# Kernel optimization log

Hardware: AMD Instinct MI355X
Metric: run time of the kernel (lower is better)

The kernel has to match this reference:

```python
import jax, jax.numpy as jnp
import numpy as np

BLOCK = 4096  # bitsandbytes blockwise-quantization block size


def setup_inputs() -> dict:
    key = jax.random.key(0)
    k_x, k_w, k_a, k_c, k_b = jax.random.split(key, 5)
    out_features, in_features = 16384, 4096
    numel = out_features * in_features
    x = jax.random.normal(k_x, (2, 2048, in_features), dtype=jnp.float32)
    # int8 codes stored as indices into the 256-entry dequant table
    qweight = jax.random.randint(k_w, (out_features, in_features), 0, 256, dtype=jnp.int32)
    absmax = jax.random.uniform(k_a, (numel // BLOCK,), dtype=jnp.float32)
    code = jax.random.normal(k_c, (256,), dtype=jnp.float32)
    bias = jax.random.normal(k_b, (out_features,), dtype=jnp.float32)
    return {"x": x, "qweight": qweight, "absmax": absmax, "code": code, "bias": bias}


def reference(x, qweight, absmax, code, bias):
    # dequantize_blockwise: w[i] = code[q[i]] * absmax[i // BLOCK]
    out_f, in_f = qweight.shape
    w = (code[qweight.reshape(-1)].reshape(-1, BLOCK) * absmax[:, None]).reshape(out_f, in_f)
    # F.linear(x, W, b) = x @ W^T + b
    return jnp.einsum("bsi,oi->bso", x, w) + bias
```

## Files before the change

kernel.cpp:

```cpp
#include <hip/hip_runtime.h>
#include <hip/hip_bf16.h>


typedef __bf16 bf16x8 __attribute__((ext_vector_type(8)));
typedef float  f32x4  __attribute__((ext_vector_type(4)));

#define GLD_LDS(gp, lp) \
    __builtin_amdgcn_global_load_lds((const __attribute__((address_space(1))) void*)(gp), \
                                     (__attribute__((address_space(3))) void*)(lp), 16, 0, 0)

static constexpr int M = 4096;
static constexpr int N = 16384;
static constexpr int K = 4096;
static constexpr int BM = 256;
static constexpr int BN = 256;
static constexpr int BK = 64;
static constexpr int NT = K / BK;
static constexpr int LDS_BYTES = 131072;

__global__ __launch_bounds__(256) void dequant_w(const int4* __restrict__ q4,
                                                 const float* __restrict__ code,
                                                 const float* __restrict__ absmax,
                                                 bf16x8* __restrict__ W)
{
    __shared__ float lc[256];
    lc[threadIdx.x] = code[threadIdx.x];
    __syncthreads();
    const unsigned total  = (unsigned)((unsigned long long)N * K / 8);
    const unsigned stride = gridDim.x * 256u;
    for (unsigned gid = blockIdx.x * 256u + threadIdx.x; gid < total; gid += stride) {
        int4 q0 = q4[2u * gid];
        int4 q1 = q4[2u * gid + 1u];
        float am = absmax[gid >> 9];
        bf16x8 w;
        w[0] = (__bf16)(lc[q0.x] * am);
        w[1] = (__bf16)(lc[q0.y] * am);
        w[2] = (__bf16)(lc[q0.z] * am);
        w[3] = (__bf16)(lc[q0.w] * am);
        w[4] = (__bf16)(lc[q1.x] * am);
        w[5] = (__bf16)(lc[q1.y] * am);
        w[6] = (__bf16)(lc[q1.z] * am);
        w[7] = (__bf16)(lc[q1.w] * am);
        W[gid] = w;
    }
}

__global__ __launch_bounds__(256) void cvt_x(const float4* __restrict__ x,
                                             bf16x8* __restrict__ xb)
{
    const unsigned total  = (unsigned)((unsigned long long)M * K / 8);
    const unsigned stride = gridDim.x * 256u;
    for (unsigned gid = blockIdx.x * 256u + threadIdx.x; gid < total; gid += stride) {
        float4 a = x[2u * gid];
        float4 b = x[2u * gid + 1u];
        bf16x8 o;
        o[0] = (__bf16)a.x; o[1] = (__bf16)a.y; o[2] = (__bf16)a.z; o[3] = (__bf16)a.w;
        o[4] = (__bf16)b.x; o[5] = (__bf16)b.y; o[6] = (__bf16)b.z; o[7] = (__bf16)b.w;
        xb[gid] = o;
    }
}


template<int MH, int NH>
__device__ __forceinline__ void mfma_quad(f32x4 (&acc)[8][4],
                                          const bf16x8 (&af)[4][2],
                                          const bf16x8 (&bf)[2][2])
{
    __builtin_amdgcn_s_setprio(1);
#pragma unroll
    for (int kk = 0; kk < 2; ++kk)
#pragma unroll
        for (int mi = 0; mi < 4; ++mi)
#pragma unroll
            for (int ni = 0; ni < 2; ++ni)
                acc[MH * 4 + mi][NH * 2 + ni] = __builtin_amdgcn_mfma_f32_16x16x32_bf16(
                    af[mi][kk], bf[ni][kk], acc[MH * 4 + mi][NH * 2 + ni], 0, 0, 0);
    __builtin_amdgcn_s_setprio(0);
}

__global__ __launch_bounds__(512, 2) void gemm_bt_bias(const __bf16* __restrict__ A,
                                                       const __bf16* __restrict__ B,
                                                       const float* __restrict__ bias,
                                                       float* __restrict__ C)
{
    extern __shared__ char lds[];
    const int tid  = threadIdx.x;
    const int lane = tid & 63;
    const int wave = tid >> 6;
    const int wm = wave >> 2;
    const int wn = wave & 3;

    const int cpx  = (int)gridDim.x >> 3;
    const int flat = ((int)blockIdx.x & 7) * cpx + ((int)blockIdx.x >> 3);
    const int bm = (flat & (M / BM - 1)) * BM;
    const int bn = (flat / (M / BM)) * BN;

    const int r0 = tid >> 3;
    const int cs = (tid & 7) ^ (r0 & 7);
    const int b_r0 = (r0 & 31) + (r0 >> 5) * 64;

    const __bf16* ag = A + (size_t)(bm + r0) * K + cs * 8;
    const __bf16* bg = B + (size_t)(bn + b_r0) * K + cs * 8;

    char* const ldsA0 = lds;
    char* const ldsB0 = lds + 32768;
    char* const ldsA1 = lds + 65536;
    char* const ldsB1 = lds + 98304;
    const int ldst = tid * 16;

    auto stageA = [&](char* dst, int h, size_t kn) {
        GLD_LDS(ag + kn + (size_t)(h * 64) * K,       dst + h * 16384 + ldst);
        GLD_LDS(ag + kn + (size_t)(h * 64 + 128) * K, dst + h * 16384 + 8192 + ldst);
    };
    auto stageB = [&](char* dst, int h, size_t kn) {
        GLD_LDS(bg + kn + (size_t)(h * 32) * K,       dst + h * 16384 + ldst);
        GLD_LDS(bg + kn + (size_t)(h * 32 + 128) * K, dst + h * 16384 + 8192 + ldst);
    };

    const int fr  = lane & 15;
    const int swz = ((lane >> 4) ^ (lane & 7)) << 4;
    const int aoff = (wm * 64 + fr) * 128 + swz;
    const int boff = (wn * 32 + fr) * 128 + swz;

    auto loadA = [&](const char* cA, int mh, bf16x8 (&af)[4][2]) {
        const int base = mh * 16384 + aoff;
#pragma unroll
        for (int mi = 0; mi < 4; ++mi) {
            af[mi][0] = *(const bf16x8*)(cA + (base + mi * 2048));
            af[mi][1] = *(const bf16x8*)(cA + ((base + mi * 2048) ^ 64));
        }
    };
    auto loadB = [&](const char* cB, int nh, bf16x8 (&bf)[2][2]) {
        const int base = nh * 16384 + boff;
#pragma unroll
        for (int ni = 0; ni < 2; ++ni) {
            bf[ni][0] = *(const bf16x8*)(cB + (base + ni * 2048));
            bf[ni][1] = *(const bf16x8*)(cB + ((base + ni * 2048) ^ 64));
        }
    };

    f32x4 acc[8][4] = {};

    stageA(ldsA0, 0, 0);
    stageB(ldsB0, 0, 0);
    stageB(ldsB0, 1, 0);
    stageA(ldsA0, 1, 0);
    asm volatile("s_waitcnt vmcnt(4)" ::: "memory");
    __builtin_amdgcn_s_barrier();

    auto tile_body = [&](const char* cA, const char* cB, char* nA, char* nB,
                         bool pf, size_t kn) {
        bf16x8 af[4][2], bf[2][2];
        if (pf) stageA(nA, 0, kn);
        loadA(cA, 0, af);
        loadB(cB, 0, bf);
        if (pf) asm volatile("s_waitcnt vmcnt(4)" ::: "memory");
        else    asm volatile("s_waitcnt vmcnt(0)" ::: "memory");
        __builtin_amdgcn_s_barrier();
        mfma_quad<0, 0>(acc, af, bf);
        if (pf) stageB(nB, 0, kn);
        loadB(cB, 1, bf);
        if (pf) {
            asm volatile("s_waitcnt vmcnt(4)" ::: "memory");
            __builtin_amdgcn_s_barrier();
        }
        mfma_quad<0, 1>(acc, af, bf);
        if (pf) stageB(nB, 1, kn);
        loadA(cA, 1, af);
        loadB(cB, 0, bf);
        if (pf) {
            asm volatile("s_waitcnt vmcnt(4)" ::: "memory");
            __builtin_amdgcn_s_barrier();
        }
        mfma_quad<1, 0>(acc, af, bf);
        if (pf) stageA(nA, 1, kn);
        loadB(cB, 1, bf);
        if (pf) {
            asm volatile("s_waitcnt vmcnt(4)" ::: "memory");
            __builtin_amdgcn_s_barrier();
        }
        mfma_quad<1, 1>(acc, af, bf);
    };

    for (int t = 0; t < NT; t += 2) {
        tile_body(ldsA0, ldsB0, ldsA1, ldsB1, true,        (size_t)(t + 1) * BK);
        tile_body(ldsA1, ldsB1, ldsA0, ldsB0, t + 2 < NT,  (size_t)(t + 2) * BK);
    }

    const int cn = lane & 15;
    const int rq = (lane >> 4) * 4;
#pragma unroll
    for (int ni = 0; ni < 4; ++ni) {
        const int n = bn + wn * 64 + ni * 16 + cn;
        const float bv = bias[n];
#pragma unroll
        for (int mi = 0; mi < 8; ++mi) {
#pragma unroll
            for (int r = 0; r < 4; ++r) {
                const int m = bm + wm * 128 + mi * 16 + rq + r;
                C[(size_t)m * N + n] = acc[mi][ni][r] + bv;
            }
        }
    }
}

extern "C" void kernel_launch(void* const* d_in, const int* in_sizes, int n_in,
                              void* d_out, int out_size, void* d_ws, size_t ws_size,
                              hipStream_t stream)
{
    const float* x      = (const float*)d_in[0];
    const int*   qw     = (const int*)d_in[1];
    const float* absmax = (const float*)d_in[2];
    const float* code   = (const float*)d_in[3];
    const float* bias   = (const float*)d_in[4];
    float* out = (float*)d_out;

    __bf16* Wb = (__bf16*)d_ws;
    __bf16* Xb = (__bf16*)((char*)d_ws + (size_t)N * K * sizeof(__bf16));

    static bool attr_set = false;
    if (!attr_set) {
        (void)hipFuncSetAttribute((const void*)gemm_bt_bias,
                                  hipFuncAttributeMaxDynamicSharedMemorySize, LDS_BYTES);
        attr_set = true;
    }

    dequant_w<<<2048, 256, 0, stream>>>((const int4*)qw, code, absmax, (bf16x8*)Wb);
    cvt_x<<<2048, 256, 0, stream>>>((const float4*)x, (bf16x8*)Xb);

    gemm_bt_bias<<<dim3((M / BM) * (N / BN)), dim3(512), LDS_BYTES, stream>>>(
        Xb, Wb, bias, out);
}
```

Measured before the change: 994.1 us.

## Restructure GEMM tile pipeline with fewer barriers and one-shot elementwise kernels

The GEMM main loop now loads all B fragments for a tile once, then iterates over A halves and k-slices issuing 16 MFMAs per group. This cuts the barriers per tile from four to two and reorders the global-to-LDS staging (B first, then A), with sched_barrier fences to pin the instruction order. The dequant and convert kernels drop their grid-stride loops in favor of one thread per 8-element chunk launched over the full problem size. Holding B fragments in registers raises register pressure, and the changed vmcnt wait counts must still cover the data each phase reads from LDS.

After: 992.6 us. No clear change (-0.2%).

```diff
diff --git a/kernel.cpp b/kernel.cpp
--- a/kernel.cpp
+++ b/kernel.cpp
@@ -26,57 +26,34 @@
     __shared__ float lc[256];
     lc[threadIdx.x] = code[threadIdx.x];
     __syncthreads();
-    const unsigned total  = (unsigned)((unsigned long long)N * K / 8);
-    const unsigned stride = gridDim.x * 256u;
-    for (unsigned gid = blockIdx.x * 256u + threadIdx.x; gid < total; gid += stride) {
-        int4 q0 = q4[2u * gid];
-        int4 q1 = q4[2u * gid + 1u];
-        float am = absmax[gid >> 9];
-        bf16x8 w;
-        w[0] = (__bf16)(lc[q0.x] * am);
-        w[1] = (__bf16)(lc[q0.y] * am);
-        w[2] = (__bf16)(lc[q0.z] * am);
-        w[3] = (__bf16)(lc[q0.w] * am);
-        w[4] = (__bf16)(lc[q1.x] * am);
-        w[5] = (__bf16)(lc[q1.y] * am);
-        w[6] = (__bf16)(lc[q1.z] * am);
-        w[7] = (__bf16)(lc[q1.w] * am);
-        W[gid] = w;
-    }
+    unsigned gid = blockIdx.x * 256u + threadIdx.x;
+    int4 q0 = q4[2u * gid];
+    int4 q1 = q4[2u * gid + 1u];
+    float am = absmax[gid >> 9];
+    bf16x8 w;
+    w[0] = (__bf16)(lc[q0.x] * am);
+    w[1] = (__bf16)(lc[q0.y] * am);
+    w[2] = (__bf16)(lc[q0.z] * am);
+    w[3] = (__bf16)(lc[q0.w] * am);
+    w[4] = (__bf16)(lc[q1.x] * am);
+    w[5] = (__bf16)(lc[q1.y] * am);
+    w[6] = (__bf16)(lc[q1.z] * am);
+    w[7] = (__bf16)(lc[q1.w] * am);
+    W[gid] = w;
 }
 
 __global__ __launch_bounds__(256) void cvt_x(const float4* __restrict__ x,
                                              bf16x8* __restrict__ xb)
 {
-    const unsigned total  = (unsigned)((unsigned long long)M * K / 8);
-    const unsigned stride = gridDim.x * 256u;
-    for (unsigned gid = blockIdx.x * 256u + threadIdx.x; gid < total; gid += stride) {
-        float4 a = x[2u * gid];
-        float4 b = x[2u * gid + 1u];
-        bf16x8 o;
-        o[0] = (__bf16)a.x; o[1] = (__bf16)a.y; o[2] = (__bf16)a.z; o[3] = (__bf16)a.w;
-        o[4] = (__bf16)b.x; o[5] = (__bf16)b.y; o[6] = (__bf16)b.z; o[7] = (__bf16)b.w;
-        xb[gid] = o;
-    }
-}
-
-
-template<int MH, int NH>
-__device__ __forceinline__ void mfma_quad(f32x4 (&acc)[8][4],
-                                          const bf16x8 (&af)[4][2],
-                                          const bf16x8 (&bf)[2][2])
-{
-    __builtin_amdgcn_s_setprio(1);
-#pragma unroll
-    for (int kk = 0; kk < 2; ++kk)
-#pragma unroll
-        for (int mi = 0; mi < 4; ++mi)
-#pragma unroll
-            for (int ni = 0; ni < 2; ++ni)
-                acc[MH * 4 + mi][NH * 2 + ni] = __builtin_amdgcn_mfma_f32_16x16x32_bf16(
-                    af[mi][kk], bf[ni][kk], acc[MH * 4 + mi][NH * 2 + ni], 0, 0, 0);
-    __builtin_amdgcn_s_setprio(0);
-}
+    unsigned gid = blockIdx.x * 256u + threadIdx.x;
+    float4 a = x[2u * gid];
+    float4 b = x[2u * gid + 1u];
+    bf16x8 o;
+    o[0] = (__bf16)a.x; o[1] = (__bf16)a.y; o[2] = (__bf16)a.z; o[3] = (__bf16)a.w;
+    o[4] = (__bf16)b.x; o[5] = (__bf16)b.y; o[6] = (__bf16)b.z; o[7] = (__bf16)b.w;
+    xb[gid] = o;
+}
+
 
 __global__ __launch_bounds__(512, 2) void gemm_bt_bias(const __bf16* __restrict__ A,
                                                        const __bf16* __restrict__ B,
@@ -122,69 +99,73 @@
     const int aoff = (wm * 64 + fr) * 128 + swz;
     const int boff = (wn * 32 + fr) * 128 + swz;
 
-    auto loadA = [&](const char* cA, int mh, bf16x8 (&af)[4][2]) {
+    auto loadA = [&](const char* cA, int mh, int kk, bf16x8 (&af)[4]) {
         const int base = mh * 16384 + aoff;
 #pragma unroll
-        for (int mi = 0; mi < 4; ++mi) {
-            af[mi][0] = *(const bf16x8*)(cA + (base + mi * 2048));
-            af[mi][1] = *(const bf16x8*)(cA + ((base + mi * 2048) ^ 64));
-        }
-    };
-    auto loadB = [&](const char* cB, int nh, bf16x8 (&bf)[2][2]) {
-        const int base = nh * 16384 + boff;
-#pragma unroll
-        for (int ni = 0; ni < 2; ++ni) {
-            bf[ni][0] = *(const bf16x8*)(cB + (base + ni * 2048));
-            bf[ni][1] = *(const bf16x8*)(cB + ((base + ni * 2048) ^ 64));
-        }
+        for (int mi = 0; mi < 4; ++mi)
+            af[mi] = *(const bf16x8*)(cA + ((base + mi * 2048) ^ (kk << 6)));
+    };
+    auto loadB = [&](const char* cB, bf16x8 (&bf)[4][2]) {
+#pragma unroll
+        for (int nh = 0; nh < 2; ++nh)
+#pragma unroll
+            for (int ni2 = 0; ni2 < 2; ++ni2) {
+                const int base = nh * 16384 + boff + ni2 * 2048;
+                bf[nh * 2 + ni2][0] = *(const bf16x8*)(cB + base);
+                bf[nh * 2 + ni2][1] = *(const bf16x8*)(cB + (base ^ 64));
+            }
     };
 
     f32x4 acc[8][4] = {};
 
-    stageA(ldsA0, 0, 0);
+    auto mfma16 = [&](int mh, int kk, const bf16x8 (&af)[4], const bf16x8 (&bf)[4][2]) {
+        __builtin_amdgcn_s_setprio(1);
+#pragma unroll
+        for (int mi = 0; mi < 4; ++mi)
+#pragma unroll
+            for (int ni = 0; ni < 4; ++ni)
+                acc[mh * 4 + mi][ni] = __builtin_amdgcn_mfma_f32_16x16x32_bf16(
+                    af[mi], bf[ni][kk], acc[mh * 4 + mi][ni], 0, 0, 0);
+        __builtin_amdgcn_s_setprio(0);
+    };
+
     stageB(ldsB0, 0, 0);
     stageB(ldsB0, 1, 0);
+    stageA(ldsA0, 0, 0);
     stageA(ldsA0, 1, 0);
-    asm volatile("s_waitcnt vmcnt(4)" ::: "memory");
+    asm volatile("s_waitcnt vmcnt(2)" ::: "memory");
     __builtin_amdgcn_s_barrier();
+    __builtin_amdgcn_sched_barrier(0);
 
     auto tile_body = [&](const char* cA, const char* cB, char* nA, char* nB,
                          bool pf, size_t kn) {
-        bf16x8 af[4][2], bf[2][2];
-        if (pf) stageA(nA, 0, kn);
-        loadA(cA, 0, af);
-        loadB(cB, 0, bf);
+        bf16x8 bf[4][2], af[4];
+        if (pf) stageB(nB, 0, kn);
+        loadB(cB, bf);
+        loadA(cA, 0, 0, af);
+        mfma16(0, 0, af, bf);
+        if (pf) stageB(nB, 1, kn);
+        loadA(cA, 0, 1, af);
+        mfma16(0, 1, af, bf);
         if (pf) asm volatile("s_waitcnt vmcnt(4)" ::: "memory");
         else    asm volatile("s_waitcnt vmcnt(0)" ::: "memory");
         __builtin_amdgcn_s_barrier();
-        mfma_quad<0, 0>(acc, af, bf);
-        if (pf) stageB(nB, 0, kn);
-        loadB(cB, 1, bf);
-        if (pf) {
-            asm volatile("s_waitcnt vmcnt(4)" ::: "memory");
-            __builtin_amdgcn_s_barrier();
-        }
-        mfma_quad<0, 1>(acc, af, bf);
-        if (pf) stageB(nB, 1, kn);
-        loadA(cA, 1, af);
-        loadB(cB, 0, bf);
-        if (pf) {
-            asm volatile("s_waitcnt vmcnt(4)" ::: "memory");
-            __builtin_amdgcn_s_barrier();
-        }
-        mfma_quad<1, 0>(acc, af, bf);
+        __builtin_amdgcn_sched_barrier(0);
+        if (pf) stageA(nA, 0, kn);
+        loadA(cA, 1, 0, af);
+        mfma16(1, 0, af, bf);
         if (pf) stageA(nA, 1, kn);
-        loadB(cB, 1, bf);
-        if (pf) {
-            asm volatile("s_waitcnt vmcnt(4)" ::: "memory");
-            __builtin_amdgcn_s_barrier();
-        }
-        mfma_quad<1, 1>(acc, af, bf);
+        loadA(cA, 1, 1, af);
+        mfma16(1, 1, af, bf);
+        if (pf) asm volatile("s_waitcnt vmcnt(2)" ::: "memory");
+        else    asm volatile("s_waitcnt vmcnt(0)" ::: "memory");
+        __builtin_amdgcn_s_barrier();
+        __builtin_amdgcn_sched_barrier(0);
     };
 
     for (int t = 0; t < NT; t += 2) {
-        tile_body(ldsA0, ldsB0, ldsA1, ldsB1, true,        (size_t)(t + 1) * BK);
-        tile_body(ldsA1, ldsB1, ldsA0, ldsB0, t + 2 < NT,  (size_t)(t + 2) * BK);
+        tile_body(ldsA0, ldsB0, ldsA1, ldsB1, true,       (size_t)(t + 1) * BK);
+        tile_body(ldsA1, ldsB1, ldsA0, ldsB0, t + 2 < NT, (size_t)(t + 2) * BK);
     }
 
     const int cn = lane & 15;
@@ -225,8 +206,10 @@
         attr_set = true;
     }
 
-    dequant_w<<<2048, 256, 0, stream>>>((const int4*)qw, code, absmax, (bf16x8*)Wb);
-    cvt_x<<<2048, 256, 0, stream>>>((const float4*)x, (bf16x8*)Xb);
+    dequant_w<<<(int)((size_t)N * K / 8 / 256), 256, 0, stream>>>(
+        (const int4*)qw, code, absmax, (bf16x8*)Wb);
+    cvt_x<<<(int)((size_t)M * K / 8 / 256), 256, 0, stream>>>(
+        (const float4*)x, (bf16x8*)Xb);
 
     gemm_bt_bias<<<dim3((M / BM) * (N / BN)), dim3(512), LDS_BYTES, stream>>>(
         Xb, Wb, bias, out);
```
